# Performance work log

Hardware: AMD Instinct MI355X
Metric: run time of the kernel (lower is better)

## Reference

```python
import jax, jax.numpy as jnp
import numpy as np

POS_TH = 0.5
NEG_TH = 0.4
NEGPOS_RATIO = 3
BBOX_ALPHA = 1.5
CONF_ALPHA = 1.0
VAR_CXCY = 0.1
VAR_WH = 0.2
NUM_CLASSES = 41
B, P, G = 8, 100000, 16


def setup_inputs() -> dict:
    key = jax.random.key(0)
    k = jax.random.split(key, 8)
    loc_data = jax.random.normal(k[0], (B, P, 4), dtype=jnp.float32)
    conf_data = jax.random.normal(k[1], (B, P, NUM_CLASSES), dtype=jnp.float32)
    # priors in (cx, cy, w, h), normalized coords
    p_cxy = jax.random.uniform(k[2], (P, 2), minval=0.0, maxval=1.0)
    p_wh = jax.random.uniform(k[3], (P, 2), minval=0.02, maxval=0.3)
    priors = jnp.concatenate([p_cxy, p_wh], axis=1).astype(jnp.float32)
    # gt boxes in point form (x1, y1, x2, y2)
    g_cxy = jax.random.uniform(k[4], (B, G, 2), minval=0.15, maxval=0.85)
    g_wh = jax.random.uniform(k[5], (B, G, 2), minval=0.05, maxval=0.4)
    gt_boxes = jnp.concatenate([
        jnp.clip(g_cxy - g_wh / 2, 0.0, 1.0),
        jnp.clip(g_cxy + g_wh / 2, 0.0, 1.0),
    ], axis=-1).astype(jnp.float32)
    gt_labels = jax.random.randint(k[6], (B, G), 1, NUM_CLASSES)
    return {"loc_data": loc_data, "conf_data": conf_data, "priors": priors,
            "gt_boxes": gt_boxes, "gt_labels": gt_labels}


def point_form(pr):
    return jnp.concatenate([pr[:, :2] - pr[:, 2:] / 2,
                            pr[:, :2] + pr[:, 2:] / 2], axis=1)


def jaccard(a, b):
    # a: [G,4] xyxy, b: [P,4] xyxy -> [G,P]
    lt = jnp.maximum(a[:, None, :2], b[None, :, :2])
    rb = jnp.minimum(a[:, None, 2:], b[None, :, 2:])
    wh = jnp.clip(rb - lt, 0.0)
    inter = wh[..., 0] * wh[..., 1]
    area_a = ((a[:, 2] - a[:, 0]) * (a[:, 3] - a[:, 1]))[:, None]
    area_b = ((b[:, 2] - b[:, 0]) * (b[:, 3] - b[:, 1]))[None, :]
    return inter / (area_a + area_b - inter)


def encode(matched, priors):
    # matched [P,4] xyxy, priors [P,4] cxcywh -> SSD offsets with variances
    g_cxcy = ((matched[:, :2] + matched[:, 2:]) / 2 - priors[:, :2]) / (VAR_CXCY * priors[:, 2:])
    g_wh = jnp.log(jnp.clip((matched[:, 2:] - matched[:, :2]) / priors[:, 2:], 1e-8)) / VAR_WH
    return jnp.concatenate([g_cxcy, g_wh], axis=1)


def match_one(gt_box, gt_label, priors):
    # gt_box [G,4], gt_label [G], priors [P,4] -> loc_t [P,4], conf_t [P]
    pf = point_form(priors)
    ov = jaccard(gt_box, pf)                      # [G,P]
    best_truth_ov = ov.max(axis=0)                # [P]
    best_truth_idx = ov.argmax(axis=0)            # [P]
    best_prior_idx = ov.argmax(axis=1)            # [G] best prior per gt
    # force-match each gt to its best prior
    best_truth_ov = best_truth_ov.at[best_prior_idx].set(2.0)
    best_truth_idx = best_truth_idx.at[best_prior_idx].set(jnp.arange(gt_box.shape[0]))
    conf = gt_label[best_truth_idx]
    conf = jnp.where(best_truth_ov < POS_TH, -1, conf)   # neutral
    conf = jnp.where(best_truth_ov < NEG_TH, 0, conf)    # background
    loc = encode(gt_box[best_truth_idx], priors)
    return loc, conf


def reference(loc_data, conf_data, priors, gt_boxes, gt_labels):
    bsz, n_pri, n_cls = conf_data.shape
    loc_t, conf_t = jax.vmap(match_one, in_axes=(0, 0, None))(gt_boxes, gt_labels, priors)
    pos = conf_t > 0                               # [B,P]
    num_pos = pos.sum(axis=1)                      # [B]
    # pos_weights: uniform 1/num_pos per image (ones split then normalized)
    pos_w = pos.astype(loc_data.dtype) / jnp.clip(num_pos, 1).astype(loc_data.dtype)[:, None]
    # localization: weighted SmoothL1 over positives
    d = loc_data - loc_t
    sl1 = jnp.where(jnp.abs(d) < 1.0, 0.5 * d * d, jnp.abs(d) - 0.5)
    loss_B = (pos_w[..., None] * sl1).sum() * BBOX_ALPHA
    # OHEM hard negative mining on background-suppression loss
    loss_c = jax.nn.logsumexp(conf_data, axis=-1) - conf_data[..., 0]
    loss_c = jnp.where(pos | (conf_t < 0), 0.0, loss_c)
    order = jnp.argsort(-loss_c, axis=1)
    rank = jnp.argsort(order, axis=1)
    num_neg = jnp.clip(NEGPOS_RATIO * num_pos, 0, n_pri - 1)
    neg = (rank < num_neg[:, None]) & (~pos) & (conf_t >= 0)
    keep = (pos | neg).astype(conf_data.dtype)
    logp = jax.nn.log_softmax(conf_data, axis=-1)
    ce = -jnp.take_along_axis(logp, jnp.clip(conf_t, 0)[..., None], axis=-1)[..., 0]
    total_pos = jnp.clip(num_pos.sum(), 1).astype(conf_data.dtype)
    loss_C = (ce * keep).sum() * CONF_ALPHA / total_pos
    return (loss_B + loss_C) / bsz
```

## Files before the change

kernel.cpp:

```cpp
#include <hip/hip_runtime.h>
#include <stdint.h>

#define BATCH 8
#define NPRI 100000
#define NGT 16
#define NCLS 41
#define F_POS_TH 0.5f
#define F_NEG_TH 0.4f

static constexpr int TPB = 256;
static constexpr int NBIN = 4096;
static constexpr int MCHUNK = 16;
static constexpr int MLEN = (NPRI + MCHUNK - 1) / MCHUNK;

static constexpr int CTPB = 128;
static constexpr int CHUNKS = 1536;
static constexpr int GLL = CHUNKS / CTPB;
static constexpr int BLK_PER_B = 96;
static constexpr int TILES_PER_B = (NPRI + CTPB - 1) / CTPB;

static constexpr size_t OFF_KEY  = 0;
static constexpr size_t OFF_GTC  = OFF_KEY + (size_t)BATCH*NPRI*4;
static constexpr size_t OFF_HG   = OFF_GTC + BATCH*NGT*8;
static constexpr size_t OFF_NPOS = OFF_HG + (size_t)BATCH*NBIN*4;
static constexpr size_t OFF_SL1  = OFF_NPOS + BATCH*4;
static constexpr size_t OFF_CEP  = OFF_SL1  + BATCH*4;
static constexpr size_t OFF_NEG  = OFF_CEP  + BATCH*4;
static constexpr size_t OFF_FTK  = OFF_NEG  + BATCH*4;
static constexpr int ZERO_U32 = (int)((OFF_FTK + 4 - OFF_NPOS) / 4);

__device__ inline float smoothl1(float d) {
  float a = fabsf(d);
  return a < 1.f ? 0.5f * d * d : a - 0.5f;
}
__device__ inline float aload_f32(const float* p) {
  return __hip_atomic_load(p, __ATOMIC_RELAXED, __HIP_MEMORY_SCOPE_AGENT);
}
__device__ __forceinline__ void gll16(const void* gsrc, void* ldst) {
  __builtin_amdgcn_global_load_lds(
      (const __attribute__((address_space(1))) void*)gsrc,
      (__attribute__((address_space(3))) void*)ldst, 16, 0, 0);
}

__global__ void k_init(unsigned* __restrict__ z, unsigned long long* __restrict__ gtc) {
  int t = threadIdx.x;
  if (t < ZERO_U32) z[t] = 0u;
  if (t < BATCH * NGT) gtc[t] = 0xFFFFFFFFull;
}

__global__ __launch_bounds__(TPB) void k_match(const float* __restrict__ priors,
                                               const float* __restrict__ gtb,
                                               unsigned long long* __restrict__ gtc,
                                               unsigned* __restrict__ histg) {
  int bg = blockIdx.y;
  int t = threadIdx.x;
  int flat = blockIdx.y * gridDim.x + blockIdx.x;
  if (t < 16) histg[flat * 16 + t] = 0u;
  const float4 gv = ((const float4*)gtb)[bg];
  float garea = (gv.z - gv.x) * (gv.w - gv.y);
  int pend = min(NPRI, (int)(blockIdx.x + 1) * MLEN);
  unsigned long long best = 0;
  for (int p = blockIdx.x * MLEN + t; p < pend; p += TPB) {
    float4 pv = ((const float4*)priors)[p];
    float px1 = pv.x - 0.5f * pv.z, py1 = pv.y - 0.5f * pv.w;
    float px2 = pv.x + 0.5f * pv.z, py2 = pv.y + 0.5f * pv.w;
    float ix = fmaxf(fminf(px2, gv.z) - fmaxf(px1, gv.x), 0.f);
    float iy = fmaxf(fminf(py2, gv.w) - fmaxf(py1, gv.y), 0.f);
    float inter = ix * iy;
    float parea = (px2 - px1) * (py2 - py1);
    float iou = inter / (parea + garea - inter);
    unsigned long long comp = ((unsigned long long)__float_as_uint(iou) << 32)
                            | (unsigned long long)(0xFFFFFFFFu - (unsigned)p);
    best = best > comp ? best : comp;
  }
#pragma unroll
  for (int off = 32; off; off >>= 1) {
    unsigned long long o = (unsigned long long)__shfl_xor((long long)best, off, 64);
    best = best > o ? best : o;
  }
  __shared__ unsigned long long red[4];
  if ((t & 63) == 0) red[t >> 6] = best;
  __syncthreads();
  if (t == 0) {
    unsigned long long r = red[0];
    r = r > red[1] ? r : red[1];
    r = r > red[2] ? r : red[2];
    r = r > red[3] ? r : red[3];
    atomicMax(&gtc[bg], r);
  }
}

__global__ __launch_bounds__(CTPB, 2) void k_conf(
    const float* __restrict__ loc, const float* __restrict__ conf,
    const float* __restrict__ priors, const float* __restrict__ gtb,
    const int* __restrict__ gtl, const unsigned long long* __restrict__ gtc,
    unsigned* __restrict__ key, unsigned* __restrict__ histg,
    unsigned* __restrict__ npos, float* __restrict__ sl1sum, float* __restrict__ cepos) {
  __shared__ float buf[2][CHUNKS * 4];
  __shared__ unsigned hcb[NBIN];
  __shared__ float red_s[2]; __shared__ unsigned red_p[2]; __shared__ float red_c[2];
  int t = threadIdx.x;
  int b = blockIdx.x / BLK_PER_B;
  int sub = blockIdx.x % BLK_PER_B;
  const float4* conf4 = (const float4*)conf;
  const size_t bbase4 = (size_t)b * NPRI * NCLS / 4;
  const size_t maxc4 = (size_t)BATCH * NPRI * NCLS / 4 - 1;
  float acc_s = 0.f, acc_c = 0.f; unsigned acc_p = 0;

  for (int i = t; i < NBIN; i += CTPB) hcb[i] = 0u;
  __syncthreads();

  {
    size_t base4 = bbase4 + (size_t)sub * CTPB * NCLS / 4;
#pragma unroll
    for (int u = 0; u < GLL; u++) {
      size_t g4 = base4 + (unsigned)(t + u * CTPB);
      if (g4 > maxc4) g4 = maxc4;
      gll16(conf4 + g4, &buf[0][(t + u * CTPB) * 4]);
    }
  }
  int cur = 0;
  for (int tidx = sub; tidx < TILES_PER_B; tidx += BLK_PER_B) {
    int p = tidx * CTPB + t;
    bool valid = p < NPRI;
    int pc = valid ? p : NPRI - 1;
    float4 pv = ((const float4*)priors)[pc];
    float4 ld = ((const float4*)loc)[(size_t)b * NPRI + pc];
    int nxt = tidx + BLK_PER_B;
    if (nxt < TILES_PER_B) {
      size_t base4 = bbase4 + (size_t)nxt * CTPB * NCLS / 4;
#pragma unroll
      for (int u = 0; u < GLL; u++) {
        size_t g4 = base4 + (unsigned)(t + u * CTPB);
        if (g4 > maxc4) g4 = maxc4;
        gll16(conf4 + g4, &buf[cur ^ 1][(t + u * CTPB) * 4]);
      }
      asm volatile("s_waitcnt vmcnt(12)" ::: "memory");
    } else {
      asm volatile("s_waitcnt vmcnt(0)" ::: "memory");
    }
    __builtin_amdgcn_sched_barrier(0);
    __builtin_amdgcn_s_barrier();
    __builtin_amdgcn_sched_barrier(0);
    unsigned kkreg = 0u;
    if (valid) {
      float px1 = pv.x - 0.5f * pv.z, py1 = pv.y - 0.5f * pv.w;
      float px2 = pv.x + 0.5f * pv.z, py2 = pv.y + 0.5f * pv.w;
      float parea = (px2 - px1) * (py2 - py1);
      float bov = 0.f; int g = 0;
#pragma unroll
      for (int gg = 0; gg < NGT; gg++) {
        const float4 gv = ((const float4*)gtb)[b * NGT + gg];
        float ix = fmaxf(fminf(px2, gv.z) - fmaxf(px1, gv.x), 0.f);
        float iy = fmaxf(fminf(py2, gv.w) - fmaxf(py1, gv.y), 0.f);
        float inter = ix * iy;
        float garea = (gv.z - gv.x) * (gv.w - gv.y);
        float iou = inter / (parea + garea - inter);
        if (iou > bov) { bov = iou; g = gg; }
      }
      float o = bov;
#pragma unroll
      for (int gg = 0; gg < NGT; gg++) {
        unsigned long long c64 = gtc[b * NGT + gg];
        unsigned pw = 0xFFFFFFFFu - (unsigned)(c64 & 0xFFFFFFFFull);
        if ((unsigned)p == pw) { o = 2.0f; g = gg; }
      }
      int c = gtl[b * NGT + g];
      if (o < F_POS_TH) c = -1;
      if (o < F_NEG_TH) c = 0;
      const float* r = &buf[cur][t * NCLS];
      float s = 0.f, r0 = 0.f, rc = 0.f;
#pragma unroll
      for (int j = 0; j < NCLS; j++) {
        float v = r[j];
        s += __expf(v);
        if (j == 0) r0 = v;
        if (j == c) rc = v;
      }
      float lse = __logf(s);
      kkreg = (c == 0) ? __float_as_uint(lse - r0) : 0u;
      key[(size_t)b * NPRI + p] = kkreg;
      if (c > 0) {
        acc_p += 1;
        acc_c += lse - rc;
        const float4 gvb = ((const float4*)gtb)[b * NGT + g];
        float tx = ((gvb.x + gvb.z) * 0.5f - pv.x) / (0.1f * pv.z);
        float ty = ((gvb.y + gvb.w) * 0.5f - pv.y) / (0.1f * pv.w);
        float tw = __logf(fmaxf((gvb.z - gvb.x) / pv.z, 1e-8f)) / 0.2f;
        float th = __logf(fmaxf((gvb.w - gvb.y) / pv.w, 1e-8f)) / 0.2f;
        acc_s += smoothl1(ld.x - tx) + smoothl1(ld.y - ty)
               + smoothl1(ld.z - tw) + smoothl1(ld.w - th);
      }
    }
    {
      unsigned long long mz = __ballot(valid && kkreg == 0u);
      if ((t & 63) == 0 && mz) atomicAdd(&hcb[0], (unsigned)__popcll(mz));
      if (valid && kkreg != 0u) atomicAdd(&hcb[kkreg >> 20], 1u);
    }
    __builtin_amdgcn_sched_barrier(0);
    __builtin_amdgcn_s_barrier();
    __builtin_amdgcn_sched_barrier(0);
    cur ^= 1;
  }
  __syncthreads();
  for (int i = t; i < NBIN; i += CTPB) {
    unsigned v = hcb[i];
    if (v) atomicAdd(&histg[b * NBIN + i], v);
  }
  float vs = acc_s, vc = acc_c; unsigned vp = acc_p;
#pragma unroll
  for (int off = 32; off; off >>= 1) {
    vs += __shfl_down(vs, off, 64);
    vc += __shfl_down(vc, off, 64);
    vp += __shfl_down(vp, off, 64);
  }
  if ((t & 63) == 0) { red_s[t >> 6] = vs; red_c[t >> 6] = vc; red_p[t >> 6] = vp; }
  __syncthreads();
  if (t == 0) {
    float ts = red_s[0] + red_s[1];
    float tc = red_c[0] + red_c[1];
    unsigned tp = red_p[0] + red_p[1];
    if (tp) atomicAdd(&npos[b], tp);
    if (ts != 0.f) atomicAdd(&sl1sum[b], ts);
    if (tc != 0.f) atomicAdd(&cepos[b], tc);
  }
}

__global__ __launch_bounds__(1024) void k_select(
    const unsigned* __restrict__ key, const unsigned* __restrict__ histg,
    const unsigned* __restrict__ npos, const float* __restrict__ sl1sum,
    const float* __restrict__ cepos, float* __restrict__ negsum,
    unsigned* __restrict__ final_tk, float* __restrict__ out) {
  __shared__ unsigned hc[NBIN];
  __shared__ unsigned pc[256], sc[256];
  __shared__ int wA; __shared__ unsigned kexA;
  __shared__ unsigned kS, prefS;
  __shared__ float redf[16];
  int b = blockIdx.x, t = threadIdx.x;
  unsigned k0 = min(3u * npos[b], (unsigned)(NPRI - 1));
  for (int i = t; i < NBIN; i += 1024) hc[i] = histg[b * NBIN + i];
  if (t == 0) { kS = k0; prefS = 0u; wA = -1; }
  __syncthreads();
  const int iters = (NPRI + 1023) / 1024;
  for (int lvl = 0; lvl < 3; lvl++) {
    unsigned k = kS;
    if (lvl > 0) {
      for (int i = t; i < NBIN; i += 1024) hc[i] = 0u;
      if (t == 0) wA = -1;
      __syncthreads();
      int shift = (lvl == 1) ? 8 : 0;
      unsigned mask = (lvl == 1) ? 0xFFFu : 0xFFu;
      int lowcut = (lvl == 1) ? 20 : 8;
      unsigned pre = prefS >> lowcut;
      for (int n = 0; n < iters; n++) {
        int i = n * 1024 + t;
        unsigned kk = (i < NPRI) ? key[(size_t)b * NPRI + i] : 0u;
        if (i < NPRI && (kk >> lowcut) == pre)
          atomicAdd(&hc[(kk >> shift) & mask], 1u);
      }
      __syncthreads();
    }
    if (t < 256) {
      unsigned cs = 0;
#pragma unroll
      for (int u = 0; u < 16; u++) cs += hc[t * 16 + u];
      pc[t] = cs; sc[t] = cs;
    }
    __syncthreads();
    for (int off = 1; off < 256; off <<= 1) {
      unsigned v = 0;
      if (t < 256) v = (t + off < 256) ? sc[t + off] : 0u;
      __syncthreads();
      if (t < 256) sc[t] += v;
      __syncthreads();
    }
    if (t < 256) {
      unsigned excl = sc[t] - pc[t];
      if (k > 0 && excl < k && k <= excl + pc[t]) { wA = t; kexA = excl; }
    }
    __syncthreads();
    if (wA >= 0 && t < 64) {
      int w = wA; unsigned exw = kexA;
      unsigned v = (t < 16) ? hc[w * 16 + t] : 0u;
      unsigned sufv = v;
#pragma unroll
      for (int off = 1; off < 16; off <<= 1) {
        unsigned x = __shfl_down(sufv, off, 64);
        if (t + off < 16) sufv += x;
      }
      unsigned excl2 = exw + (sufv - v);
      if (t < 16 && excl2 < k && k <= excl2 + v) {
        int shift = (lvl == 0) ? 20 : (lvl == 1) ? 8 : 0;
        prefS |= ((unsigned)(w * 16 + t)) << shift;
        kS = k - excl2;
      }
    }
    __syncthreads();
  }
  unsigned Tu = prefS;
  unsigned tie = kS;
  float acc = 0.f;
  if (k0 > 0) {
    for (int n = 0; n < iters; n++) {
      int i = n * 1024 + t;
      if (i < NPRI) {
        unsigned kk = key[(size_t)b * NPRI + i];
        if (kk > Tu) acc += __uint_as_float(kk);
      }
    }
  }
#pragma unroll
  for (int off = 32; off; off >>= 1) acc += __shfl_down(acc, off, 64);
  if ((t & 63) == 0) redf[t >> 6] = acc;
  __syncthreads();
  if (t == 0) {
    float tot = 0.f;
    for (int wv = 0; wv < 16; wv++) tot += redf[wv];
    if (k0 > 0) tot += (float)tie * __uint_as_float(Tu);
    negsum[b] = tot;
    __threadfence();
    unsigned r2 = atomicAdd(final_tk, 1u);
    if (r2 == BATCH - 1) {
      __threadfence();
      float lb = 0.f, ctot = 0.f; unsigned tp = 0;
      for (int bb = 0; bb < BATCH; bb++) {
        lb += aload_f32(&sl1sum[bb]) / fmaxf((float)npos[bb], 1.f);
        tp += npos[bb];
        ctot += aload_f32(&cepos[bb]) + aload_f32(&negsum[bb]);
      }
      out[0] = (1.5f * lb + ctot / fmaxf((float)tp, 1.f)) / (float)BATCH;
      *final_tk = 0;
    }
  }
}

extern "C" void kernel_launch(void* const* d_in, const int* in_sizes, int n_in,
                              void* d_out, int out_size, void* d_ws, size_t ws_size,
                              hipStream_t stream) {
  const float* loc = (const float*)d_in[0];
  const float* conf = (const float*)d_in[1];
  const float* priors = (const float*)d_in[2];
  const float* gtb = (const float*)d_in[3];
  const int* gtl = (const int*)d_in[4];
  char* ws = (char*)d_ws;
  unsigned* key = (unsigned*)(ws + OFF_KEY);
  unsigned long long* gtc = (unsigned long long*)(ws + OFF_GTC);
  unsigned* histg = (unsigned*)(ws + OFF_HG);
  unsigned* npos = (unsigned*)(ws + OFF_NPOS);
  float* sl1sum = (float*)(ws + OFF_SL1);
  float* cepos = (float*)(ws + OFF_CEP);
  float* negsum = (float*)(ws + OFF_NEG);
  unsigned* final_tk = (unsigned*)(ws + OFF_FTK);
  float* out = (float*)d_out;

  k_init<<<1, 160, 0, stream>>>(npos, gtc);
  dim3 gridM(MCHUNK, BATCH * NGT);
  k_match<<<gridM, TPB, 0, stream>>>(priors, gtb, gtc, histg);
  k_conf<<<BATCH * BLK_PER_B, CTPB, 0, stream>>>(loc, conf, priors, gtb, gtl, gtc,
                                                 key, histg, npos, sl1sum, cepos);
  k_select<<<BATCH, 1024, 0, stream>>>(key, histg, npos, sl1sum, cepos,
                                       negsum, final_tk, out);
}
```

Baseline: 156.8 us.

## Use single-wave conf blocks and a coarse 256-bin first-level histogram

The confidence kernel now runs as single-wavefront blocks of 64 threads, 224 per image, so the block barriers around the double-buffered LDS prefetch can be dropped and the small per-block LDS footprint allows more resident blocks. The per-block histogram shrinks from 4096 to 256 bins (key top 8 bits), so clearing it and flushing it to global memory is cheaper. The select kernel's radix search changes from a 12/12/8-bit split to 8/12/12 to match. The costs are more global atomics from many more blocks and a coarser first level, which can leave more candidates for the later passes over the keys.

```diff
diff --git a/kernel.cpp b/kernel.cpp
--- a/kernel.cpp
+++ b/kernel.cpp
@@ -9,25 +9,25 @@
 #define F_NEG_TH 0.4f
 
 static constexpr int TPB = 256;
-static constexpr int NBIN = 4096;
 static constexpr int MCHUNK = 16;
 static constexpr int MLEN = (NPRI + MCHUNK - 1) / MCHUNK;
 
-static constexpr int CTPB = 128;
-static constexpr int CHUNKS = 1536;
-static constexpr int GLL = CHUNKS / CTPB;
-static constexpr int BLK_PER_B = 96;
-static constexpr int TILES_PER_B = (NPRI + CTPB - 1) / CTPB;
+static constexpr int WTPB = 64;
+static constexpr int CPT = WTPB * NCLS / 4;
+static constexpr int BLK_PER_B = 224;
+static constexpr int TILES_PER_B = (NPRI + WTPB - 1) / WTPB;
+static constexpr int H0BIN = 256;
+static constexpr int NBIN = 4096;
 
 static constexpr size_t OFF_KEY  = 0;
 static constexpr size_t OFF_GTC  = OFF_KEY + (size_t)BATCH*NPRI*4;
 static constexpr size_t OFF_HG   = OFF_GTC + BATCH*NGT*8;
-static constexpr size_t OFF_NPOS = OFF_HG + (size_t)BATCH*NBIN*4;
+static constexpr size_t OFF_NPOS = OFF_HG + (size_t)BATCH*H0BIN*4;
 static constexpr size_t OFF_SL1  = OFF_NPOS + BATCH*4;
 static constexpr size_t OFF_CEP  = OFF_SL1  + BATCH*4;
 static constexpr size_t OFF_NEG  = OFF_CEP  + BATCH*4;
 static constexpr size_t OFF_FTK  = OFF_NEG  + BATCH*4;
-static constexpr int ZERO_U32 = (int)((OFF_FTK + 4 - OFF_NPOS) / 4);
+static constexpr int ZERO_U32 = (int)((OFF_FTK + 4 - OFF_HG) / 4);
 
 __device__ inline float smoothl1(float d) {
   float a = fabsf(d);
@@ -44,18 +44,15 @@
 
 __global__ void k_init(unsigned* __restrict__ z, unsigned long long* __restrict__ gtc) {
   int t = threadIdx.x;
-  if (t < ZERO_U32) z[t] = 0u;
+  for (int i = t; i < ZERO_U32; i += 512) z[i] = 0u;
   if (t < BATCH * NGT) gtc[t] = 0xFFFFFFFFull;
 }
 
 __global__ __launch_bounds__(TPB) void k_match(const float* __restrict__ priors,
                                                const float* __restrict__ gtb,
-                                               unsigned long long* __restrict__ gtc,
-                                               unsigned* __restrict__ histg) {
+                                               unsigned long long* __restrict__ gtc) {
   int bg = blockIdx.y;
   int t = threadIdx.x;
-  int flat = blockIdx.y * gridDim.x + blockIdx.x;
-  if (t < 16) histg[flat * 16 + t] = 0u;
   const float4 gv = ((const float4*)gtb)[bg];
   float garea = (gv.z - gv.x) * (gv.w - gv.y);
   int pend = min(NPRI, (int)(blockIdx.x + 1) * MLEN);
@@ -90,15 +87,14 @@
   }
 }
 
-__global__ __launch_bounds__(CTPB, 2) void k_conf(
+__global__ __launch_bounds__(WTPB) void k_conf(
     const float* __restrict__ loc, const float* __restrict__ conf,
     const float* __restrict__ priors, const float* __restrict__ gtb,
     const int* __restrict__ gtl, const unsigned long long* __restrict__ gtc,
     unsigned* __restrict__ key, unsigned* __restrict__ histg,
     unsigned* __restrict__ npos, float* __restrict__ sl1sum, float* __restrict__ cepos) {
-  __shared__ float buf[2][CHUNKS * 4];
-  __shared__ unsigned hcb[NBIN];
-  __shared__ float red_s[2]; __shared__ unsigned red_p[2]; __shared__ float red_c[2];
+  __shared__ float buf[2][CPT * 4];
+  __shared__ unsigned hcb[H0BIN];
   int t = threadIdx.x;
   int b = blockIdx.x / BLK_PER_B;
   int sub = blockIdx.x % BLK_PER_B;
@@ -106,41 +102,48 @@
   const size_t bbase4 = (size_t)b * NPRI * NCLS / 4;
   const size_t maxc4 = (size_t)BATCH * NPRI * NCLS / 4 - 1;
   float acc_s = 0.f, acc_c = 0.f; unsigned acc_p = 0;
-
-  for (int i = t; i < NBIN; i += CTPB) hcb[i] = 0u;
-  __syncthreads();
+#pragma unroll
+  for (int u = 0; u < H0BIN / WTPB; u++) hcb[t + u * WTPB] = 0u;
 
   {
-    size_t base4 = bbase4 + (size_t)sub * CTPB * NCLS / 4;
-#pragma unroll
-    for (int u = 0; u < GLL; u++) {
-      size_t g4 = base4 + (unsigned)(t + u * CTPB);
+    size_t base4 = bbase4 + (size_t)sub * CPT;
+#pragma unroll
+    for (int u = 0; u < 10; u++) {
+      size_t g4 = base4 + (unsigned)(t + u * WTPB);
       if (g4 > maxc4) g4 = maxc4;
-      gll16(conf4 + g4, &buf[0][(t + u * CTPB) * 4]);
+      gll16(conf4 + g4, &buf[0][(t + u * WTPB) * 4]);
+    }
+    if (t < CPT - 10 * WTPB) {
+      size_t g4 = base4 + (unsigned)(t + 10 * WTPB);
+      if (g4 > maxc4) g4 = maxc4;
+      gll16(conf4 + g4, &buf[0][(t + 10 * WTPB) * 4]);
     }
   }
   int cur = 0;
   for (int tidx = sub; tidx < TILES_PER_B; tidx += BLK_PER_B) {
-    int p = tidx * CTPB + t;
+    int p = tidx * WTPB + t;
     bool valid = p < NPRI;
     int pc = valid ? p : NPRI - 1;
     float4 pv = ((const float4*)priors)[pc];
     float4 ld = ((const float4*)loc)[(size_t)b * NPRI + pc];
     int nxt = tidx + BLK_PER_B;
     if (nxt < TILES_PER_B) {
-      size_t base4 = bbase4 + (size_t)nxt * CTPB * NCLS / 4;
-#pragma unroll
-      for (int u = 0; u < GLL; u++) {
-        size_t g4 = base4 + (unsigned)(t + u * CTPB);
+      size_t base4 = bbase4 + (size_t)nxt * CPT;
+#pragma unroll
+      for (int u = 0; u < 10; u++) {
+        size_t g4 = base4 + (unsigned)(t + u * WTPB);
         if (g4 > maxc4) g4 = maxc4;
-        gll16(conf4 + g4, &buf[cur ^ 1][(t + u * CTPB) * 4]);
-      }
-      asm volatile("s_waitcnt vmcnt(12)" ::: "memory");
+        gll16(conf4 + g4, &buf[cur ^ 1][(t + u * WTPB) * 4]);
+      }
+      if (t < CPT - 10 * WTPB) {
+        size_t g4 = base4 + (unsigned)(t + 10 * WTPB);
+        if (g4 > maxc4) g4 = maxc4;
+        gll16(conf4 + g4, &buf[cur ^ 1][(t + 10 * WTPB) * 4]);
+      }
+      asm volatile("s_waitcnt vmcnt(11)" ::: "memory");
     } else {
       asm volatile("s_waitcnt vmcnt(0)" ::: "memory");
     }
-    __builtin_amdgcn_sched_barrier(0);
-    __builtin_amdgcn_s_barrier();
     __builtin_amdgcn_sched_barrier(0);
     unsigned kkreg = 0u;
     if (valid) {
@@ -180,6 +183,7 @@
       float lse = __logf(s);
       kkreg = (c == 0) ? __float_as_uint(lse - r0) : 0u;
       key[(size_t)b * NPRI + p] = kkreg;
+      atomicAdd(&hcb[kkreg >> 24], 1u);
       if (c > 0) {
         acc_p += 1;
         acc_c += lse - rc;
@@ -192,20 +196,12 @@
                + smoothl1(ld.z - tw) + smoothl1(ld.w - th);
       }
     }
-    {
-      unsigned long long mz = __ballot(valid && kkreg == 0u);
-      if ((t & 63) == 0 && mz) atomicAdd(&hcb[0], (unsigned)__popcll(mz));
-      if (valid && kkreg != 0u) atomicAdd(&hcb[kkreg >> 20], 1u);
-    }
-    __builtin_amdgcn_sched_barrier(0);
-    __builtin_amdgcn_s_barrier();
-    __builtin_amdgcn_sched_barrier(0);
     cur ^= 1;
   }
-  __syncthreads();
-  for (int i = t; i < NBIN; i += CTPB) {
-    unsigned v = hcb[i];
-    if (v) atomicAdd(&histg[b * NBIN + i], v);
+#pragma unroll
+  for (int u = 0; u < H0BIN / WTPB; u++) {
+    unsigned v = hcb[t + u * WTPB];
+    if (v) atomicAdd(&histg[b * H0BIN + t + u * WTPB], v);
   }
   float vs = acc_s, vc = acc_c; unsigned vp = acc_p;
 #pragma unroll
@@ -214,15 +210,10 @@
     vc += __shfl_down(vc, off, 64);
     vp += __shfl_down(vp, off, 64);
   }
-  if ((t & 63) == 0) { red_s[t >> 6] = vs; red_c[t >> 6] = vc; red_p[t >> 6] = vp; }
-  __syncthreads();
   if (t == 0) {
-    float ts = red_s[0] + red_s[1];
-    float tc = red_c[0] + red_c[1];
-    unsigned tp = red_p[0] + red_p[1];
-    if (tp) atomicAdd(&npos[b], tp);
-    if (ts != 0.f) atomicAdd(&sl1sum[b], ts);
-    if (tc != 0.f) atomicAdd(&cepos[b], tc);
+    if (vp) atomicAdd(&npos[b], vp);
+    if (vs != 0.f) atomicAdd(&sl1sum[b], vs);
+    if (vc != 0.f) atomicAdd(&cepos[b], vc);
   }
 }
 
@@ -232,39 +223,53 @@
     const float* __restrict__ cepos, float* __restrict__ negsum,
     unsigned* __restrict__ final_tk, float* __restrict__ out) {
   __shared__ unsigned hc[NBIN];
-  __shared__ unsigned pc[256], sc[256];
+  __shared__ unsigned pcs[256], sc[256];
   __shared__ int wA; __shared__ unsigned kexA;
   __shared__ unsigned kS, prefS;
   __shared__ float redf[16];
   int b = blockIdx.x, t = threadIdx.x;
   unsigned k0 = min(3u * npos[b], (unsigned)(NPRI - 1));
-  for (int i = t; i < NBIN; i += 1024) hc[i] = histg[b * NBIN + i];
-  if (t == 0) { kS = k0; prefS = 0u; wA = -1; }
-  __syncthreads();
   const int iters = (NPRI + 1023) / 1024;
-  for (int lvl = 0; lvl < 3; lvl++) {
+  if (t < 256) { unsigned v = histg[b * H0BIN + t]; pcs[t] = v; sc[t] = v; }
+  if (t == 0) { kS = 0u; prefS = 0u; wA = -1; }
+  __syncthreads();
+  for (int off = 1; off < 256; off <<= 1) {
+    unsigned v = 0;
+    if (t < 256) v = (t + off < 256) ? sc[t + off] : 0u;
+    __syncthreads();
+    if (t < 256) sc[t] += v;
+    __syncthreads();
+  }
+  if (t < 256) {
+    unsigned excl = sc[t] - pcs[t];
+    if (k0 > 0 && excl < k0 && k0 <= excl + pcs[t]) { wA = t; kexA = excl; }
+  }
+  __syncthreads();
+  if (t == 0 && wA >= 0) { prefS = ((unsigned)wA) << 24; kS = k0 - kexA; }
+  __syncthreads();
+  for (int lvl = 1; lvl <= 2; lvl++) {
     unsigned k = kS;
-    if (lvl > 0) {
-      for (int i = t; i < NBIN; i += 1024) hc[i] = 0u;
-      if (t == 0) wA = -1;
-      __syncthreads();
-      int shift = (lvl == 1) ? 8 : 0;
-      unsigned mask = (lvl == 1) ? 0xFFFu : 0xFFu;
-      int lowcut = (lvl == 1) ? 20 : 8;
-      unsigned pre = prefS >> lowcut;
+    int shift = (lvl == 1) ? 12 : 0;
+    int lowcut = (lvl == 1) ? 24 : 12;
+    for (int i = t; i < NBIN; i += 1024) hc[i] = 0u;
+    if (t == 0) wA = -1;
+    __syncthreads();
+    unsigned pre = prefS >> lowcut;
+    if (k > 0) {
       for (int n = 0; n < iters; n++) {
         int i = n * 1024 + t;
-        unsigned kk = (i < NPRI) ? key[(size_t)b * NPRI + i] : 0u;
-        if (i < NPRI && (kk >> lowcut) == pre)
-          atomicAdd(&hc[(kk >> shift) & mask], 1u);
-      }
-      __syncthreads();
-    }
+        if (i < NPRI) {
+          unsigned kk = key[(size_t)b * NPRI + i];
+          if ((kk >> lowcut) == pre) atomicAdd(&hc[(kk >> shift) & 0xFFFu], 1u);
+        }
+      }
+    }
+    __syncthreads();
     if (t < 256) {
       unsigned cs = 0;
 #pragma unroll
       for (int u = 0; u < 16; u++) cs += hc[t * 16 + u];
-      pc[t] = cs; sc[t] = cs;
+      pcs[t] = cs; sc[t] = cs;
     }
     __syncthreads();
     for (int off = 1; off < 256; off <<= 1) {
@@ -275,8 +280,8 @@
       __syncthreads();
     }
     if (t < 256) {
-      unsigned excl = sc[t] - pc[t];
-      if (k > 0 && excl < k && k <= excl + pc[t]) { wA = t; kexA = excl; }
+      unsigned excl = sc[t] - pcs[t];
+      if (k > 0 && excl < k && k <= excl + pcs[t]) { wA = t; kexA = excl; }
     }
     __syncthreads();
     if (wA >= 0 && t < 64) {
@@ -290,7 +295,6 @@
       }
       unsigned excl2 = exw + (sufv - v);
       if (t < 16 && excl2 < k && k <= excl2 + v) {
-        int shift = (lvl == 0) ? 20 : (lvl == 1) ? 8 : 0;
         prefS |= ((unsigned)(w * 16 + t)) << shift;
         kS = k - excl2;
       }
@@ -353,10 +357,10 @@
   unsigned* final_tk = (unsigned*)(ws + OFF_FTK);
   float* out = (float*)d_out;
 
-  k_init<<<1, 160, 0, stream>>>(npos, gtc);
+  k_init<<<1, 512, 0, stream>>>(histg, gtc);
   dim3 gridM(MCHUNK, BATCH * NGT);
-  k_match<<<gridM, TPB, 0, stream>>>(priors, gtb, gtc, histg);
-  k_conf<<<BATCH * BLK_PER_B, CTPB, 0, stream>>>(loc, conf, priors, gtb, gtl, gtc,
+  k_match<<<gridM, TPB, 0, stream>>>(priors, gtb, gtc);
+  k_conf<<<BATCH * BLK_PER_B, WTPB, 0, stream>>>(loc, conf, priors, gtb, gtl, gtc,
                                                  key, histg, npos, sl1sum, cepos);
   k_select<<<BATCH, 1024, 0, stream>>>(key, histg, npos, sl1sum, cepos,
                                        negsum, final_tk, out);
```

New measurement: 151.3 us. 1.04x faster.
